# Optimization experiments

Hardware: AMD Instinct MI355X
Metric: run time of the kernel (lower is better)

The kernel has to match this reference:

```python
import jax, jax.numpy as jnp
import numpy as np

B = 4000        # graphs
N = 64          # atoms (nodes) per graph; also conv1 in_channels (Linear(num_atoms, 64))
C = 64          # hidden / out channels (hard-coded 64 in ChargeModel)
E_PER = 512     # edges per graph (avg degree 8)
NT = B * N      # total nodes


def setup_inputs() -> dict:
    key = jax.random.key(0)
    ks = jax.random.split(key, 10)
    x = jax.random.normal(ks[0], (NT, N), dtype=jnp.float32)
    # block-local random edges: each graph's edges stay inside its node block
    off = (jnp.arange(B, dtype=jnp.int32) * N)[:, None]
    src = (jax.random.randint(ks[1], (B, E_PER), 0, N, dtype=jnp.int32) + off).reshape(-1)
    dst = (jax.random.randint(ks[2], (B, E_PER), 0, N, dtype=jnp.int32) + off).reshape(-1)
    edge_index = jnp.stack([src, dst], axis=0)  # [2, B*E_PER]
    s = 1.0 / jnp.sqrt(jnp.float32(C))  # keep activations O(1) across 3 layers
    W1 = jax.random.normal(ks[3], (N, C), dtype=jnp.float32) * s
    W2 = jax.random.normal(ks[4], (C, C), dtype=jnp.float32) * s
    W3 = jax.random.normal(ks[5], (C, C), dtype=jnp.float32) * s
    b1 = jax.random.normal(ks[6], (C,), dtype=jnp.float32) * 0.1
    b2 = jax.random.normal(ks[7], (C,), dtype=jnp.float32) * 0.1
    b3 = jax.random.normal(ks[8], (C,), dtype=jnp.float32) * 0.1
    return {"x": x, "edge_index": edge_index, "W1": W1, "b1": b1,
            "W2": W2, "b2": b2, "W3": W3, "b3": b3}


def reference(x, edge_index, W1, b1, W2, b2, W3, b3):
    nt = x.shape[0]
    src, dst = edge_index[0], edge_index[1]
    loops = jnp.arange(nt, dtype=src.dtype)
    row = jnp.concatenate([src, loops])  # self-loops appended (add_self_loops)
    col = jnp.concatenate([dst, loops])
    # degree of target nodes (col), shared across the three layers
    deg = jax.ops.segment_sum(jnp.ones(row.shape[0], dtype=x.dtype), col, num_segments=nt)
    dinv = jnp.where(deg > 0, jax.lax.rsqrt(jnp.maximum(deg, 1e-12)), 0.0)
    norm = dinv[row] * dinv[col]  # [E']

    def gcn(h, W, b):
        h = h @ W                                   # linear (no bias in lin)
        msg = norm[:, None] * h[row]                # message: norm * x_j
        out = jax.ops.segment_sum(msg, col, num_segments=nt)  # aggr='add'
        return out + b

    h = gcn(x, W1, b1)
    h = gcn(h, W2, b2)
    h = gcn(h, W3, b3)
    # per-graph readout: mean over nodes and channels -> one scalar per graph
    y = h.reshape(B, N, C).mean(axis=(1, 2))
    return y
```

## Files before the change

kernel.cpp:

```cpp
#include <hip/hip_runtime.h>

#define NG      4000
#define EPG     512
#define CSTRIDE 35

__device__ inline float dot4(const float4 a, const float4 b) {
    return a.x * b.x + a.y * b.y + a.z * b.z + a.w * b.w;
}

__global__ __launch_bounds__(256) void prep_vec(
    const float* __restrict__ W1, const float* __restrict__ b1,
    const float* __restrict__ W2, const float* __restrict__ b2,
    const float* __restrict__ W3, const float* __restrict__ b3,
    float* __restrict__ out)
{
    __shared__ float w3[64], q2[64];
    const int t  = threadIdx.x;
    const int rg = t >> 4;
    const int l16 = t & 15;

    const float4* W1_4 = (const float4*)W1;
    const float4* W2_4 = (const float4*)W2;
    const float4* W3_4 = (const float4*)W3;
    float4 a3[4], a2[4], a1[4];
    #pragma unroll
    for (int j = 0; j < 4; ++j) a3[j] = W3_4[t + 256 * j];
    #pragma unroll
    for (int j = 0; j < 4; ++j) a2[j] = W2_4[t + 256 * j];
    #pragma unroll
    for (int j = 0; j < 4; ++j) a1[j] = W1_4[t + 256 * j];
    float bb1 = 0.f, bb2 = 0.f, bb3 = 0.f;
    if (t < 64) { bb1 = b1[t]; bb2 = b2[t]; bb3 = b3[t]; }

    #pragma unroll
    for (int j = 0; j < 4; ++j) {
        float s = a3[j].x + a3[j].y + a3[j].z + a3[j].w;
        s += __shfl_down(s, 8, 16);
        s += __shfl_down(s, 4, 16);
        s += __shfl_down(s, 2, 16);
        s += __shfl_down(s, 1, 16);
        if (l16 == 0) w3[16 * j + rg] = s;
    }
    __syncthreads();

    {
        const float4 wc = ((const float4*)w3)[l16];
        #pragma unroll
        for (int j = 0; j < 4; ++j) {
            float s = dot4(a2[j], wc);
            s += __shfl_down(s, 8, 16);
            s += __shfl_down(s, 4, 16);
            s += __shfl_down(s, 2, 16);
            s += __shfl_down(s, 1, 16);
            if (l16 == 0) q2[16 * j + rg] = s;
        }
    }
    __syncthreads();

    {
        const float4 qc = ((const float4*)q2)[l16];
        #pragma unroll
        for (int j = 0; j < 4; ++j) {
            float s = dot4(a1[j], qc);
            s += __shfl_down(s, 8, 16);
            s += __shfl_down(s, 4, 16);
            s += __shfl_down(s, 2, 16);
            s += __shfl_down(s, 1, 16);
            if (l16 == 0) out[16 * j + rg] = s;
        }
    }

    if (t < 64) {
        float t1 = bb1 * q2[t];
        float t2 = bb2 * w3[t];
        float t3 = bb3;
        #pragma unroll
        for (int off = 32; off > 0; off >>= 1) {
            t1 += __shfl_down(t1, off, 64);
            t2 += __shfl_down(t2, off, 64);
            t3 += __shfl_down(t3, off, 64);
        }
        if (t == 0) { out[64] = t1; out[65] = t2; out[66] = 64.f * t3; }
    }
}

__global__ __launch_bounds__(256, 8) void gcn3_collapse2(
    const float* __restrict__ x, const int* __restrict__ ei,
    const float* __restrict__ pv, float* __restrict__ y, int etot)
{
    __shared__ int   Cnt[64 * CSTRIDE];
    __shared__ int   deg4[4][64];
    __shared__ float dinv[64], zdA[64], zdB[64], u1[64], u2[64], u3[64], xp[64];

    const int g = blockIdx.x, t = threadIdx.x;
    const int w = t >> 6;
    const int base = g * 64;
    const int row = t >> 2, q4 = t & 3;

    const float4* xg = (const float4*)(x + (size_t)g * 4096 + row * 64 + q4 * 16);
    const float4 xr0 = xg[0], xr1 = xg[1], xr2 = xg[2], xr3 = xg[3];

    const int2 sv = *(const int2*)(ei + (size_t)g * EPG + 2 * t);
    const int2 dv = *(const int2*)(ei + (size_t)etot + (size_t)g * EPG + 2 * t);

    const float4* pp = (const float4*)(pv + q4 * 16);
    const float4 p0 = pp[0], p1 = pp[1], p2 = pp[2], p3 = pp[3];

    {
        const int4 z = {0, 0, 0, 0};
        int4* c4 = (int4*)Cnt;
        #pragma unroll 1
        for (int i = t; i < (64 * CSTRIDE) / 4; i += 256) c4[i] = z;
        ((int*)deg4)[t] = 0;
    }
    __syncthreads();

    {
        const int sa = sv.x - base, da = dv.x - base;
        const int sb = sv.y - base, db = dv.y - base;
        atomicAdd(&deg4[w][da], 1);
        atomicAdd(&deg4[w][db], 1);
        atomicAdd(&Cnt[sa * CSTRIDE + (da >> 1)], 1 << ((da & 1) * 16));
        atomicAdd(&Cnt[sb * CSTRIDE + (db >> 1)], 1 << ((db & 1) * 16));
    }

    {
        float part = dot4(xr0, p0) + dot4(xr1, p1) + dot4(xr2, p2) + dot4(xr3, p3);
        part += __shfl_down(part, 2, 4);
        part += __shfl_down(part, 1, 4);
        if (q4 == 0) xp[row] = part;
    }
    __syncthreads();

    if (t < 64) {
        const int ds = deg4[0][t] + deg4[1][t] + deg4[2][t] + deg4[3][t];
        const float di = rsqrtf((float)(ds + 1));
        dinv[t] = di;
        zdA[t] = di;
    }
    __syncthreads();

    auto upass = [&](const float* zin, float* zout, const float* uprev, float* u) {
        const int* rp = Cnt + row * CSTRIDE + q4 * 8;
        float acc = 0.f;
        #pragma unroll
        for (int i = 0; i < 8; ++i) {
            const unsigned v = (unsigned)rp[i];
            const int d0 = q4 * 16 + 2 * i;
            acc += (float)(v & 0xffffu) * zin[d0];
            acc += (float)(v >> 16)     * zin[d0 + 1];
        }
        acc += __shfl_down(acc, 2, 4);
        acc += __shfl_down(acc, 1, 4);
        if (q4 == 0) {
            const float di = dinv[row];
            const float zp = uprev ? uprev[row] : 1.0f;
            const float uv = di * acc + di * di * zp;
            u[row] = uv;
            if (zout) zout[row] = di * uv;
        }
        __syncthreads();
    };

    upass(zdA, zdB, nullptr, u1);
    upass(zdB, zdA, u1,      u2);
    upass(zdA, nullptr, u2,  u3);

    if (t < 64) {
        float r  = u3[t] * xp[t];
        float a1 = u1[t];
        float a2 = u2[t];
        #pragma unroll
        for (int off = 32; off > 0; off >>= 1) {
            r  += __shfl_down(r,  off, 64);
            a1 += __shfl_down(a1, off, 64);
            a2 += __shfl_down(a2, off, 64);
        }
        if (t == 0) {
            const float beta1 = pv[64], beta2 = pv[65], beta3 = pv[66];
            y[g] = (r + a2 * beta1 + a1 * beta2 + beta3) * (1.0f / 4096.0f);
        }
    }
}

extern "C" void kernel_launch(void* const* d_in, const int* in_sizes, int n_in,
                              void* d_out, int out_size, void* d_ws, size_t ws_size,
                              hipStream_t stream) {
    const float* x  = (const float*)d_in[0];
    const int*   ei = (const int*)  d_in[1];
    const float* W1 = (const float*)d_in[2];
    const float* b1 = (const float*)d_in[3];
    const float* W2 = (const float*)d_in[4];
    const float* b2 = (const float*)d_in[5];
    const float* W3 = (const float*)d_in[6];
    const float* b3 = (const float*)d_in[7];
    float* y = (float*)d_out;
    const int etot = in_sizes[1] / 2;

    float* pv = (float*)d_ws;
    hipLaunchKernelGGL(prep_vec, dim3(1), dim3(256), 0, stream,
                       W1, b1, W2, b2, W3, b3, pv);
    hipLaunchKernelGGL(gcn3_collapse2, dim3(NG), dim3(256), 0, stream,
                       x, ei, pv, y, etot);
}
```

Baseline: 23.45 us.

## Replace packed adjacency-count matrix with per-layer float atomic edge scatter

Drops the 64x35 shared count matrix that was built with packed 16-bit atomics and swept three times. Each of the three propagation passes now scatters the edge messages straight into a 64-float shared accumulator with float atomicAdd. This removes the matrix zeroing and the dense sweeps and cuts shared memory use. In exchange it adds three rounds of float LDS atomics, which can contend on the same destination node, plus extra barriers. Float accumulation order becomes nondeterministic.

Measured after the change: 47.06 us. 2.01x slower.

```diff
diff --git a/kernel.cpp b/kernel.cpp
--- a/kernel.cpp
+++ b/kernel.cpp
@@ -1,8 +1,7 @@
 #include <hip/hip_runtime.h>
 
-#define NG      4000
-#define EPG     512
-#define CSTRIDE 35
+#define NG   4000
+#define EPG  512
 
 __device__ inline float dot4(const float4 a, const float4 b) {
     return a.x * b.x + a.y * b.y + a.z * b.z + a.w * b.w;
@@ -84,45 +83,39 @@
     }
 }
 
-__global__ __launch_bounds__(256, 8) void gcn3_collapse2(
+__global__ __launch_bounds__(256, 8) void gcn3_scatter(
     const float* __restrict__ x, const int* __restrict__ ei,
     const float* __restrict__ pv, float* __restrict__ y, int etot)
 {
-    __shared__ int   Cnt[64 * CSTRIDE];
     __shared__ int   deg4[4][64];
-    __shared__ float dinv[64], zdA[64], zdB[64], u1[64], u2[64], u3[64], xp[64];
+    __shared__ float accA[64], accB[64], accC[64];
+    __shared__ float zdA[64], zdB[64];
+    __shared__ float dinvS[64], xp[64];
 
     const int g = blockIdx.x, t = threadIdx.x;
-    const int w = t >> 6;
+    const int w = t >> 6, lane = t & 63;
     const int base = g * 64;
     const int row = t >> 2, q4 = t & 3;
 
+    const int2 sv = *(const int2*)(ei + (size_t)g * EPG + 2 * t);
+    const int2 dv = *(const int2*)(ei + (size_t)etot + (size_t)g * EPG + 2 * t);
+
     const float4* xg = (const float4*)(x + (size_t)g * 4096 + row * 64 + q4 * 16);
     const float4 xr0 = xg[0], xr1 = xg[1], xr2 = xg[2], xr3 = xg[3];
 
-    const int2 sv = *(const int2*)(ei + (size_t)g * EPG + 2 * t);
-    const int2 dv = *(const int2*)(ei + (size_t)etot + (size_t)g * EPG + 2 * t);
-
     const float4* pp = (const float4*)(pv + q4 * 16);
     const float4 p0 = pp[0], p1 = pp[1], p2 = pp[2], p3 = pp[3];
 
-    {
-        const int4 z = {0, 0, 0, 0};
-        int4* c4 = (int4*)Cnt;
-        #pragma unroll 1
-        for (int i = t; i < (64 * CSTRIDE) / 4; i += 256) c4[i] = z;
-        ((int*)deg4)[t] = 0;
-    }
-    __syncthreads();
-
-    {
-        const int sa = sv.x - base, da = dv.x - base;
-        const int sb = sv.y - base, db = dv.y - base;
-        atomicAdd(&deg4[w][da], 1);
-        atomicAdd(&deg4[w][db], 1);
-        atomicAdd(&Cnt[sa * CSTRIDE + (da >> 1)], 1 << ((da & 1) * 16));
-        atomicAdd(&Cnt[sb * CSTRIDE + (db >> 1)], 1 << ((db & 1) * 16));
-    }
+    deg4[w][lane] = 0;
+    if (w == 1) accA[lane] = 0.f;
+    if (w == 2) accB[lane] = 0.f;
+    if (w == 3) accC[lane] = 0.f;
+
+    const int sa = sv.x - base, da = dv.x - base;
+    const int sb = sv.y - base, db = dv.y - base;
+
+    atomicAdd(&deg4[w][da], 1);
+    atomicAdd(&deg4[w][db], 1);
 
     {
         float part = dot4(xr0, p0) + dot4(xr1, p1) + dot4(xr2, p2) + dot4(xr3, p3);
@@ -132,44 +125,46 @@
     }
     __syncthreads();
 
+    float di = 0.f;
     if (t < 64) {
         const int ds = deg4[0][t] + deg4[1][t] + deg4[2][t] + deg4[3][t];
-        const float di = rsqrtf((float)(ds + 1));
-        dinv[t] = di;
+        di = rsqrtf((float)(ds + 1));
+        dinvS[t] = di;
         zdA[t] = di;
     }
     __syncthreads();
 
-    auto upass = [&](const float* zin, float* zout, const float* uprev, float* u) {
-        const int* rp = Cnt + row * CSTRIDE + q4 * 8;
-        float acc = 0.f;
-        #pragma unroll
-        for (int i = 0; i < 8; ++i) {
-            const unsigned v = (unsigned)rp[i];
-            const int d0 = q4 * 16 + 2 * i;
-            acc += (float)(v & 0xffffu) * zin[d0];
-            acc += (float)(v >> 16)     * zin[d0 + 1];
-        }
-        acc += __shfl_down(acc, 2, 4);
-        acc += __shfl_down(acc, 1, 4);
-        if (q4 == 0) {
-            const float di = dinv[row];
-            const float zp = uprev ? uprev[row] : 1.0f;
-            const float uv = di * acc + di * di * zp;
-            u[row] = uv;
-            if (zout) zout[row] = di * uv;
-        }
-        __syncthreads();
-    };
-
-    upass(zdA, zdB, nullptr, u1);
-    upass(zdB, zdA, u1,      u2);
-    upass(zdA, nullptr, u2,  u3);
-
-    if (t < 64) {
-        float r  = u3[t] * xp[t];
-        float a1 = u1[t];
-        float a2 = u2[t];
+    atomicAdd(&accA[sa], zdA[da]);
+    atomicAdd(&accA[sb], zdA[db]);
+    __syncthreads();
+
+    float u1 = 0.f;
+    if (t < 64) {
+        u1 = di * accA[t] + di * di;
+        zdB[t] = di * u1;
+    }
+    __syncthreads();
+
+    atomicAdd(&accB[sa], zdB[da]);
+    atomicAdd(&accB[sb], zdB[db]);
+    __syncthreads();
+
+    float u2 = 0.f;
+    if (t < 64) {
+        u2 = di * accB[t] + di * di * u1;
+        zdA[t] = di * u2;
+    }
+    __syncthreads();
+
+    atomicAdd(&accC[sa], zdA[da]);
+    atomicAdd(&accC[sb], zdA[db]);
+    __syncthreads();
+
+    if (t < 64) {
+        const float u3 = di * accC[t] + di * di * u2;
+        float r  = u3 * xp[t];
+        float a1 = u1;
+        float a2 = u2;
         #pragma unroll
         for (int off = 32; off > 0; off >>= 1) {
             r  += __shfl_down(r,  off, 64);
@@ -200,6 +195,6 @@
     float* pv = (float*)d_ws;
     hipLaunchKernelGGL(prep_vec, dim3(1), dim3(256), 0, stream,
                        W1, b1, W2, b2, W3, b3, pv);
-    hipLaunchKernelGGL(gcn3_collapse2, dim3(NG), dim3(256), 0, stream,
+    hipLaunchKernelGGL(gcn3_scatter, dim3(NG), dim3(256), 0, stream,
                        x, ei, pv, y, etot);
 }
```

## Run the three propagation passes in a single wavefront using shuffles

Applied to the files above, without the earlier changes.

After the counts are built, the three upass stages no longer use all four wavefronts with shared-memory vectors and block barriers. Only wavefront 0 continues. Each lane loads its full count row into registers as int4 and broadcasts z values with __shfl, so the three dependent passes need no __syncthreads. The count row stride becomes 36 so rows are 16-byte aligned for int4 loads, and the zeroing loop is unrolled. The trade-off is serial work on one wave (64 shuffles per pass) and possible LDS bank conflicts from the stride-36 row loads.

New measurement: 37.84 us. +61.4%, slower.

```diff
diff --git a/kernel.cpp b/kernel.cpp
--- a/kernel.cpp
+++ b/kernel.cpp
@@ -2,7 +2,7 @@
 
 #define NG      4000
 #define EPG     512
-#define CSTRIDE 35
+#define CSTRIDE 36
 
 __device__ inline float dot4(const float4 a, const float4 b) {
     return a.x * b.x + a.y * b.y + a.z * b.z + a.w * b.w;
@@ -84,16 +84,16 @@
     }
 }
 
-__global__ __launch_bounds__(256, 8) void gcn3_collapse2(
+__global__ __launch_bounds__(256, 8) void gcn3_shflchain(
     const float* __restrict__ x, const int* __restrict__ ei,
     const float* __restrict__ pv, float* __restrict__ y, int etot)
 {
     __shared__ int   Cnt[64 * CSTRIDE];
     __shared__ int   deg4[4][64];
-    __shared__ float dinv[64], zdA[64], zdB[64], u1[64], u2[64], u3[64], xp[64];
+    __shared__ float xp[64];
 
     const int g = blockIdx.x, t = threadIdx.x;
-    const int w = t >> 6;
+    const int w = t >> 6, lane = t & 63;
     const int base = g * 64;
     const int row = t >> 2, q4 = t & 3;
 
@@ -109,8 +109,8 @@
     {
         const int4 z = {0, 0, 0, 0};
         int4* c4 = (int4*)Cnt;
-        #pragma unroll 1
-        for (int i = t; i < (64 * CSTRIDE) / 4; i += 256) c4[i] = z;
+        c4[t] = z; c4[t + 256] = z;
+        if (t < 64) c4[t + 512] = z;
         ((int*)deg4)[t] = 0;
     }
     __syncthreads();
@@ -132,54 +132,57 @@
     }
     __syncthreads();
 
-    if (t < 64) {
-        const int ds = deg4[0][t] + deg4[1][t] + deg4[2][t] + deg4[3][t];
-        const float di = rsqrtf((float)(ds + 1));
-        dinv[t] = di;
-        zdA[t] = di;
-    }
-    __syncthreads();
-
-    auto upass = [&](const float* zin, float* zout, const float* uprev, float* u) {
-        const int* rp = Cnt + row * CSTRIDE + q4 * 8;
-        float acc = 0.f;
-        #pragma unroll
-        for (int i = 0; i < 8; ++i) {
-            const unsigned v = (unsigned)rp[i];
-            const int d0 = q4 * 16 + 2 * i;
-            acc += (float)(v & 0xffffu) * zin[d0];
-            acc += (float)(v >> 16)     * zin[d0 + 1];
-        }
-        acc += __shfl_down(acc, 2, 4);
-        acc += __shfl_down(acc, 1, 4);
-        if (q4 == 0) {
-            const float di = dinv[row];
-            const float zp = uprev ? uprev[row] : 1.0f;
-            const float uv = di * acc + di * di * zp;
-            u[row] = uv;
-            if (zout) zout[row] = di * uv;
-        }
-        __syncthreads();
-    };
-
-    upass(zdA, zdB, nullptr, u1);
-    upass(zdB, zdA, u1,      u2);
-    upass(zdA, nullptr, u2,  u3);
-
-    if (t < 64) {
-        float r  = u3[t] * xp[t];
-        float a1 = u1[t];
-        float a2 = u2[t];
-        #pragma unroll
-        for (int off = 32; off > 0; off >>= 1) {
-            r  += __shfl_down(r,  off, 64);
-            a1 += __shfl_down(a1, off, 64);
-            a2 += __shfl_down(a2, off, 64);
-        }
-        if (t == 0) {
-            const float beta1 = pv[64], beta2 = pv[65], beta3 = pv[66];
-            y[g] = (r + a2 * beta1 + a1 * beta2 + beta3) * (1.0f / 4096.0f);
-        }
+    if (w != 0) return;
+
+    int4 cr[8];
+    {
+        const int4* rp = (const int4*)(Cnt + lane * CSTRIDE);
+        #pragma unroll
+        for (int j = 0; j < 8; ++j) cr[j] = rp[j];
+    }
+    const int ds = deg4[0][lane] + deg4[1][lane] + deg4[2][lane] + deg4[3][lane];
+    const float dz = rsqrtf((float)(ds + 1));
+
+    const int* cri = (const int*)cr;
+
+    float zcur = dz;
+    float uprev = 1.f;
+    float u1 = 0.f, u2 = 0.f, u3 = 0.f;
+
+    #pragma unroll
+    for (int pass = 0; pass < 3; ++pass) {
+        float a0 = 0.f, a1_ = 0.f, a2_ = 0.f, a3_ = 0.f;
+        #pragma unroll
+        for (int d = 0; d < 64; d += 4) {
+            const float zb0 = __shfl(zcur, d + 0, 64);
+            const float zb1 = __shfl(zcur, d + 1, 64);
+            const float zb2 = __shfl(zcur, d + 2, 64);
+            const float zb3 = __shfl(zcur, d + 3, 64);
+            const int v0 = cri[(d >> 1)];
+            const int v1 = cri[(d >> 1) + 1];
+            a0 += (float)((unsigned)v0 & 0xffffu) * zb0;
+            a1_ += (float)((unsigned)v0 >> 16)     * zb1;
+            a2_ += (float)((unsigned)v1 & 0xffffu) * zb2;
+            a3_ += (float)((unsigned)v1 >> 16)     * zb3;
+        }
+        const float acc = (a0 + a1_) + (a2_ + a3_);
+        const float u = dz * acc + dz * dz * uprev;
+        if (pass == 0) u1 = u; else if (pass == 1) u2 = u; else u3 = u;
+        uprev = u;
+        zcur = dz * u;
+    }
+
+    float r  = u3 * xp[lane];
+    float a1 = u1, a2 = u2;
+    #pragma unroll
+    for (int off = 32; off > 0; off >>= 1) {
+        r  += __shfl_down(r,  off, 64);
+        a1 += __shfl_down(a1, off, 64);
+        a2 += __shfl_down(a2, off, 64);
+    }
+    if (lane == 0) {
+        const float beta1 = pv[64], beta2 = pv[65], beta3 = pv[66];
+        y[g] = (r + a2 * beta1 + a1 * beta2 + beta3) * (1.0f / 4096.0f);
     }
 }
 
@@ -200,6 +203,6 @@
     float* pv = (float*)d_ws;
     hipLaunchKernelGGL(prep_vec, dim3(1), dim3(256), 0, stream,
                        W1, b1, W2, b2, W3, b3, pv);
-    hipLaunchKernelGGL(gcn3_collapse2, dim3(NG), dim3(256), 0, stream,
+    hipLaunchKernelGGL(gcn3_shflchain, dim3(NG), dim3(256), 0, stream,
                        x, ei, pv, y, etot);
 }
```
